# Kernel optimization log

Hardware: AMD Instinct MI355X
Metric: run time of the kernel (lower is better)

The kernel has to match this reference:

```python
import jax, jax.numpy as jnp
import numpy as np

B, N, D_IN, D_OUT = 8, 2048, 256, 128
ROW_ZERO = 85 - 10  # hardcoded in original: a[:, 0:85-10] = 0 (zeros rows, dim 1)
NEG_BIG = -9.0e15
EPS = 1e-12  # F.normalize eps


def setup_inputs() -> dict:
    key = jax.random.key(0)
    k1, k2, k3, k4 = jax.random.split(key, 4)
    h = jax.random.normal(k1, (B, N, D_IN), dtype=jnp.float32)
    adj = jax.random.randint(k2, (B, N, N), 0, 2, dtype=jnp.int32)
    adj_eye = jax.random.randint(k3, (B, N, N), 0, 2, dtype=jnp.int32)
    # xavier_uniform with gain=1.414 for W [in, out]
    limit = 1.414 * np.sqrt(6.0 / (D_IN + D_OUT))
    W = jax.random.uniform(k4, (D_IN, D_OUT), minval=-limit, maxval=limit, dtype=jnp.float32)
    return {"h": h, "adj": adj, "adj_eye": adj_eye, "W": W}


def reference(h, adj, adj_eye, W):
    # Wh: [B, N, D_OUT]
    Wh = jnp.matmul(h, W)
    # L2-normalize along feature dim (F.normalize semantics: x / max(||x||, eps))
    norm = jnp.maximum(jnp.linalg.norm(Wh, axis=-1, keepdims=True), EPS)
    Whn = Wh / norm
    # dense cosine-similarity scores: [B, N, N]
    score = jnp.einsum("bnd,bmd->bnm", Whn, Whn)
    # double-sort top-k emulation (faithful to original, incl. row-wise zeroing bug)
    a_sorted = jnp.sort(score, axis=-1)
    idx1 = jnp.argsort(score, axis=-1)
    a_sorted = a_sorted.at[:, 0:ROW_ZERO, :].set(0.0)
    idx2 = jnp.argsort(idx1, axis=-1)  # inverse permutation
    attscore = jnp.take_along_axis(a_sorted, idx2, axis=-1)
    # adjacency mask + softmax over neighbors
    e = jnp.where(adj_eye > 0, attscore, NEG_BIG)
    attention = jax.nn.softmax(e, axis=-1)
    # (dropout is identity in eval mode)
    h_prime = jnp.matmul(attention, Wh)
    return jax.nn.elu(h_prime)
```

## Files before the change

kernel.cpp:

```cpp
#include <hip/hip_runtime.h>
#include <stdint.h>

#define NN   2048
#define DD   128
#define DIN  256
#define ROWZ 75

typedef float f32x4 __attribute__((ext_vector_type(4)));
typedef short bf16x8 __attribute__((ext_vector_type(8)));
typedef unsigned int u32x4 __attribute__((ext_vector_type(4)));
typedef unsigned int u32x2 __attribute__((ext_vector_type(2)));
typedef unsigned long long u64x2 __attribute__((ext_vector_type(2)));

__device__ __forceinline__ unsigned short f2bf(float x){
  union { float f; unsigned int u; } v; v.f = x;
  unsigned int u = v.u;
  u += 0x7fffu + ((u >> 16) & 1u);
  return (unsigned short)(u >> 16);
}
__device__ __forceinline__ float bf2f(unsigned short b){
  union { float f; unsigned int u; } v; v.u = ((unsigned int)b) << 16;
  return v.f;
}

__launch_bounds__(256, 8)
__global__ void pack_kernel(const int* __restrict__ adje,
                            unsigned long long* __restrict__ adjp)
{
  const int t  = threadIdx.x;
  const int wv = t >> 6;
  const int ln = t & 63;
#pragma unroll
  for (int rr = 0; rr < 2; ++rr){
    const int row = blockIdx.x * 8 + wv * 2 + rr;
    const int* arow = adje + (size_t)row * NN;
    unsigned long long* drow = adjp + (size_t)row * 32;
#pragma unroll
    for (int c = 0; c < 4; ++c){
      int pv[8];
#pragma unroll
      for (int j = 0; j < 8; ++j) pv[j] = arow[c*512 + j*64 + ln];
      unsigned long long m[8];
#pragma unroll
      for (int j = 0; j < 8; ++j) m[j] = __ballot(pv[j] > 0);
      if (ln == 0){
#pragma unroll
        for (int j = 0; j < 8; j += 2){
          u64x2 pk = { m[j], m[j+1] };
          *(u64x2*)(drow + c*8 + j) = pk;
        }
      }
    }
  }
}

__launch_bounds__(256, 2)
__global__ void wh_kernel(const float* __restrict__ h, const float* __restrict__ W,
                          unsigned short* __restrict__ whn, unsigned short* __restrict__ whT)
{
  __shared__ float hs[32][36];
  __shared__ float Ws[32][128];
  __shared__ float ssp[32][33];
  __shared__ float sinv[32];

  const int t  = threadIdx.x;
  const int r0 = blockIdx.x * 32;
  const int r4 = (t >> 5) * 4;
  const int d4 = (t & 31) * 4;

  float acc[4][4];
#pragma unroll
  for (int i = 0; i < 4; ++i)
#pragma unroll
    for (int j = 0; j < 4; ++j) acc[i][j] = 0.f;

  const int lrow = t >> 3;
  const int lkb  = (t & 7) * 4;
  const int wk   = t >> 3;
  const int wd   = (t & 7) * 16;

  f32x4 ph = *(const f32x4*)(h + (size_t)(r0 + lrow) * DIN + lkb);
  f32x4 pW[4];
  {
    const float* ws = W + (size_t)wk * DD + wd;
#pragma unroll
    for (int e = 0; e < 4; ++e) pW[e] = ((const f32x4*)ws)[e];
  }

  for (int kt = 0; kt < 8; ++kt){
    __syncthreads();
#pragma unroll
    for (int e = 0; e < 4; ++e) hs[lkb + e][lrow] = ph[e];
    {
      f32x4* dst = (f32x4*)&Ws[wk][wd];
#pragma unroll
      for (int e = 0; e < 4; ++e) dst[e] = pW[e];
    }
    __syncthreads();

    if (kt < 7){
      ph = *(const f32x4*)(h + (size_t)(r0 + lrow) * DIN + (kt+1)*32 + lkb);
      const float* ws = W + (size_t)((kt+1)*32 + wk) * DD + wd;
#pragma unroll
      for (int e = 0; e < 4; ++e) pW[e] = ((const f32x4*)ws)[e];
    }

#pragma unroll
    for (int k = 0; k < 32; ++k){
      f32x4 w4 = *(const f32x4*)&Ws[k][d4];
      f32x4 ha = *(const f32x4*)&hs[k][r4];
#pragma unroll
      for (int i = 0; i < 4; ++i)
#pragma unroll
        for (int j = 0; j < 4; ++j)
          acc[i][j] += ha[i] * w4[j];
    }
  }

#pragma unroll
  for (int i = 0; i < 4; ++i){
    float s = acc[i][0]*acc[i][0] + acc[i][1]*acc[i][1]
            + acc[i][2]*acc[i][2] + acc[i][3]*acc[i][3];
    ssp[r4 + i][t & 31] = s;
  }
  __syncthreads();
  if (t < 32){
    float ss = 0.f;
#pragma unroll
    for (int c = 0; c < 32; ++c) ss += ssp[t][c];
    sinv[t] = 1.0f / fmaxf(sqrtf(ss), 1e-12f);
  }
  __syncthreads();

  const int bb = r0 >> 11;
  const int n0 = (r0 & 2047) + r4;

#pragma unroll
  for (int i = 0; i < 4; ++i){
    const float inv = sinv[r4 + i];
    unsigned int lo = (unsigned int)f2bf(acc[i][0]*inv) | ((unsigned int)f2bf(acc[i][1]*inv) << 16);
    unsigned int hi = (unsigned int)f2bf(acc[i][2]*inv) | ((unsigned int)f2bf(acc[i][3]*inv) << 16);
    u32x2 pk = { lo, hi };
    *(u32x2*)(whn + (size_t)(r0 + r4 + i) * DD + d4) = pk;
  }
#pragma unroll
  for (int j = 0; j < 4; ++j){
    u32x2 pk;
#pragma unroll
    for (int e = 0; e < 2; ++e)
      pk[e] = (unsigned int)f2bf(acc[2*e][j]) | ((unsigned int)f2bf(acc[2*e + 1][j]) << 16);
    *(u32x2*)(whT + ((size_t)(bb * DD + d4 + j)) * NN + n0) = pk;
  }
}

__launch_bounds__(256, 2)
__global__ void attn_kernel(const unsigned short* __restrict__ whn,
                            const unsigned short* __restrict__ whT,
                            const unsigned int* __restrict__ adjp,
                            float* __restrict__ out)
{
  __shared__ unsigned short Vt[2][128 * 128];
  __shared__ unsigned short Pbuf[4][32 * 40];
  __shared__ float linv_s[32];

  const int t    = threadIdx.x;
  const int w    = t >> 6;
  const int l    = t & 63;
  const int quad = l >> 4;
  const int l16  = l & 15;
  const int b     = blockIdx.x & 7;
  const int qbase = (blockIdx.x >> 3) * 32;

  const unsigned short* whn_b = whn + (size_t)b * NN * DD;
  const unsigned short* whT_b = whT + (size_t)b * DD * NN;
  const unsigned int*   adjw  = adjp + ((size_t)(b * NN + qbase)) * 64;

  bf16x8 qf[2][4];
#pragma unroll
  for (int s = 0; s < 2; ++s)
#pragma unroll
    for (int kc = 0; kc < 4; ++kc)
      qf[s][kc] = *(const bf16x8*)(whn_b + (size_t)(qbase + s*16 + l16) * DD + kc*32 + quad*8);

  f32x4 oacc[2][8];
  float lacc[2][4];
#pragma unroll
  for (int s = 0; s < 2; ++s){
#pragma unroll
    for (int dt = 0; dt < 8; ++dt) oacc[s][dt] = (f32x4){0.f, 0.f, 0.f, 0.f};
#pragma unroll
    for (int r = 0; r < 4; ++r) lacc[s][r] = 0.f;
  }

  unsigned short* const Pw = &Pbuf[w][0];

#pragma unroll
  for (int ii = 0; ii < 8; ++ii){
    const int d   = w*32 + ii*4 + quad;
    const int gsw = l16 ^ (d & 7);
    const unsigned short* src = whT_b + (size_t)d * NN + gsw * 8;
    __builtin_amdgcn_global_load_lds(
        (const __attribute__((address_space(1))) void*)src,
        (__attribute__((address_space(3))) void*)&Vt[0][(w*32 + ii*4) * 128],
        16, 0, 0);
  }
  unsigned int aw[2][4];
#pragma unroll
  for (int s = 0; s < 2; ++s)
#pragma unroll
    for (int r = 0; r < 4; ++r)
      aw[s][r] = adjw[(size_t)(s*16 + quad*4 + r) * 64 + w];

  for (int it = 0; it < 16; ++it){
    const int m0  = it * 128;
    const int cur = it & 1;

    bf16x8 kf[2][4];
#pragma unroll
    for (int f = 0; f < 2; ++f)
#pragma unroll
      for (int kc = 0; kc < 4; ++kc)
        kf[f][kc] = *(const bf16x8*)(whn_b + (size_t)(m0 + w*32 + f*16 + l16) * DD + kc*32 + quad*8);

    unsigned int awn[2][4];
    if (it < 15){
#pragma unroll
      for (int s = 0; s < 2; ++s)
#pragma unroll
        for (int r = 0; r < 4; ++r)
          awn[s][r] = adjw[(size_t)(s*16 + quad*4 + r) * 64 + (it+1)*4 + w];
#pragma unroll
      for (int ii = 0; ii < 8; ++ii){
        const int d   = w*32 + ii*4 + quad;
        const int gsw = l16 ^ (d & 7);
        const unsigned short* src = whT_b + (size_t)d * NN + (m0 + 128) + gsw * 8;
        __builtin_amdgcn_global_load_lds(
            (const __attribute__((address_space(1))) void*)src,
            (__attribute__((address_space(3))) void*)&Vt[cur ^ 1][(w*32 + ii*4) * 128],
            16, 0, 0);
      }
    }

#pragma unroll
    for (int f = 0; f < 2; ++f){
#pragma unroll
      for (int s = 0; s < 2; ++s){
        f32x4 sc = (f32x4){0.f, 0.f, 0.f, 0.f};
#pragma unroll
        for (int kc = 0; kc < 4; ++kc)
          sc = __builtin_amdgcn_mfma_f32_16x16x32_bf16(qf[s][kc], kf[f][kc], sc, 0, 0, 0);
#pragma unroll
        for (int r = 0; r < 4; ++r){
          const int qrow = qbase + s*16 + quad*4 + r;
          float sv = (qrow < ROWZ) ? 0.f : sc[r];
          float p32 = ((aw[s][r] >> (f*16 + l16)) & 1u) ? __expf(sv) : 0.f;
          unsigned short pb = f2bf(p32);
          lacc[s][r] += bf2f(pb);
          Pw[(s*16 + quad*4 + r) * 40 + f*16 + l16] = pb;
        }
      }
    }

    __builtin_amdgcn_sched_barrier(0);
    __builtin_amdgcn_s_barrier();
    __builtin_amdgcn_sched_barrier(0);

    bf16x8 pfr0 = *(const bf16x8*)&Pw[(l16) * 40 + quad*8];
    bf16x8 pfr1 = *(const bf16x8*)&Pw[(16 + l16) * 40 + quad*8];
    __builtin_amdgcn_s_setprio(1);
#pragma unroll
    for (int dt = 0; dt < 8; ++dt){
      const int d  = dt*16 + l16;
      const int gg = (w*4 + quad) ^ (d & 7);
      bf16x8 vf = *(const bf16x8*)&Vt[cur][d * 128 + gg * 8];
      oacc[0][dt] = __builtin_amdgcn_mfma_f32_16x16x32_bf16(pfr0, vf, oacc[0][dt], 0, 0, 0);
      oacc[1][dt] = __builtin_amdgcn_mfma_f32_16x16x32_bf16(pfr1, vf, oacc[1][dt], 0, 0, 0);
    }
    __builtin_amdgcn_s_setprio(0);

    __builtin_amdgcn_sched_barrier(0);
    __builtin_amdgcn_s_barrier();
    __builtin_amdgcn_sched_barrier(0);

    if (it < 15){
#pragma unroll
      for (int s = 0; s < 2; ++s)
#pragma unroll
        for (int r = 0; r < 4; ++r)
          aw[s][r] = awn[s][r];
    }
  }

  {
    float* lredw = (float*)Pw;
#pragma unroll
    for (int s = 0; s < 2; ++s)
#pragma unroll
      for (int r = 0; r < 4; ++r)
        lredw[(s*16 + quad*4 + r) * 16 + l16] = lacc[s][r];
  }
  __syncthreads();
  if (t < 32){
    float sum = 0.f;
    for (int ww = 0; ww < 4; ++ww){
      const float* lr = (const float*)&Pbuf[ww][0];
#pragma unroll
      for (int c = 0; c < 16; ++c) sum += lr[t * 16 + c];
    }
    linv_s[t] = 1.0f / sum;
  }

  float* const ored = (float*)&Vt[0][0];
  for (int s = 0; s < 2; ++s){
    __syncthreads();
#pragma unroll
    for (int dt = 0; dt < 8; ++dt)
#pragma unroll
      for (int r = 0; r < 4; ++r)
        ored[w*2048 + (quad*4 + r)*128 + dt*16 + l16] = oacc[s][dt][r];
    __syncthreads();
#pragma unroll
    for (int j = 0; j < 8; ++j){
      const int o  = j*256 + t;
      const int ql = o >> 7, d = o & 127;
      float v = ored[ql*128 + d] + ored[2048 + ql*128 + d]
              + ored[4096 + ql*128 + d] + ored[6144 + ql*128 + d];
      v *= linv_s[s*16 + ql];
      v = (v > 0.f) ? v : expm1f(v);
      out[(size_t)(b*NN + qbase + s*16 + ql) * DD + d] = v;
    }
  }
}

extern "C" void kernel_launch(void* const* d_in, const int* in_sizes, int n_in,
                              void* d_out, int out_size, void* d_ws, size_t ws_size,
                              hipStream_t stream)
{
  const float* h       = (const float*)d_in[0];
  const int*   adj_eye = (const int*)d_in[2];
  const float* W       = (const float*)d_in[3];
  float*       out     = (float*)d_out;

  unsigned short* whn  = (unsigned short*)d_ws;
  unsigned short* whT  = whn + (size_t)16384 * 128;
  unsigned int*   adjp = (unsigned int*)(whT + (size_t)16384 * 128);

  pack_kernel<<<2048, 256, 0, stream>>>(adj_eye, (unsigned long long*)adjp);
  wh_kernel<<<512, 256, 0, stream>>>(h, W, whn, whT);
  attn_kernel<<<512, 256, 0, stream>>>(whn, whT, adjp, out);
}
```

Before: 329.8 us.

## Fuse adjacency packing into attention kernel and stage K tiles in LDS

Drops the separate pack kernel; the attention kernel now reads the int32 adjacency directly, prefetching it one tile ahead in registers. Blocks grow to 512 threads covering 64 query rows, with half the waves staging K tiles and half staging V tiles into double-buffered LDS through direct global-to-LDS loads. The wh kernel's block-to-row mapping is interleaved across batches. The aim is to remove a kernel launch and the write and reread of a packed bitmask, and to share K/V tiles across more query rows. In exchange each block reads 4-byte adjacency values instead of packed bits, and the larger LDS footprint may lower occupancy.

```diff
diff --git a/kernel.cpp b/kernel.cpp
--- a/kernel.cpp
+++ b/kernel.cpp
@@ -8,9 +8,7 @@
 
 typedef float f32x4 __attribute__((ext_vector_type(4)));
 typedef short bf16x8 __attribute__((ext_vector_type(8)));
-typedef unsigned int u32x4 __attribute__((ext_vector_type(4)));
 typedef unsigned int u32x2 __attribute__((ext_vector_type(2)));
-typedef unsigned long long u64x2 __attribute__((ext_vector_type(2)));
 
 __device__ __forceinline__ unsigned short f2bf(float x){
   union { float f; unsigned int u; } v; v.f = x;
@@ -21,37 +19,6 @@
 __device__ __forceinline__ float bf2f(unsigned short b){
   union { float f; unsigned int u; } v; v.u = ((unsigned int)b) << 16;
   return v.f;
-}
-
-__launch_bounds__(256, 8)
-__global__ void pack_kernel(const int* __restrict__ adje,
-                            unsigned long long* __restrict__ adjp)
-{
-  const int t  = threadIdx.x;
-  const int wv = t >> 6;
-  const int ln = t & 63;
-#pragma unroll
-  for (int rr = 0; rr < 2; ++rr){
-    const int row = blockIdx.x * 8 + wv * 2 + rr;
-    const int* arow = adje + (size_t)row * NN;
-    unsigned long long* drow = adjp + (size_t)row * 32;
-#pragma unroll
-    for (int c = 0; c < 4; ++c){
-      int pv[8];
-#pragma unroll
-      for (int j = 0; j < 8; ++j) pv[j] = arow[c*512 + j*64 + ln];
-      unsigned long long m[8];
-#pragma unroll
-      for (int j = 0; j < 8; ++j) m[j] = __ballot(pv[j] > 0);
-      if (ln == 0){
-#pragma unroll
-        for (int j = 0; j < 8; j += 2){
-          u64x2 pk = { m[j], m[j+1] };
-          *(u64x2*)(drow + c*8 + j) = pk;
-        }
-      }
-    }
-  }
 }
 
 __launch_bounds__(256, 2)
@@ -64,7 +31,8 @@
   __shared__ float sinv[32];
 
   const int t  = threadIdx.x;
-  const int r0 = blockIdx.x * 32;
+  const int bid = blockIdx.x;
+  const int r0 = ((bid & 7) << 11) | ((bid >> 3) << 5);
   const int r4 = (t >> 5) * 4;
   const int d4 = (t & 31) * 4;
 
@@ -153,34 +121,62 @@
   }
 }
 
-__launch_bounds__(256, 2)
+__launch_bounds__(512, 2)
 __global__ void attn_kernel(const unsigned short* __restrict__ whn,
                             const unsigned short* __restrict__ whT,
-                            const unsigned int* __restrict__ adjp,
+                            const int* __restrict__ adje,
                             float* __restrict__ out)
 {
+  __shared__ unsigned short Kt[2][128 * 128];
   __shared__ unsigned short Vt[2][128 * 128];
-  __shared__ unsigned short Pbuf[4][32 * 40];
-  __shared__ float linv_s[32];
+  __shared__ unsigned short Pbuf[8][32 * 40];
+  __shared__ float linv_s[64];
 
   const int t    = threadIdx.x;
   const int w    = t >> 6;
   const int l    = t & 63;
   const int quad = l >> 4;
   const int l16  = l & 15;
+  const int qh   = w >> 2;
+  const int ms   = w & 3;
   const int b     = blockIdx.x & 7;
-  const int qbase = (blockIdx.x >> 3) * 32;
+  const int qbase = (blockIdx.x >> 3) * 64;
 
   const unsigned short* whn_b = whn + (size_t)b * NN * DD;
   const unsigned short* whT_b = whT + (size_t)b * DD * NN;
-  const unsigned int*   adjw  = adjp + ((size_t)(b * NN + qbase)) * 64;
+  const int*            adj_b = adje + (size_t)b * NN * NN;
+
+#define STAGE(M0, CC)                                                          \
+  if (w < 4){                                                                  \
+    _Pragma("unroll")                                                          \
+    for (int ii = 0; ii < 8; ++ii){                                            \
+      const int row = w*32 + ii*4 + (l >> 4);                                  \
+      const unsigned short* src = whn_b + (size_t)((M0) + row) * DD            \
+                                  + (l16 ^ (row & 7)) * 8;                     \
+      __builtin_amdgcn_global_load_lds(                                        \
+          (const __attribute__((address_space(1))) void*)src,                  \
+          (__attribute__((address_space(3))) void*)&Kt[CC][(w*32 + ii*4)*128], \
+          16, 0, 0);                                                           \
+    }                                                                          \
+  } else {                                                                     \
+    _Pragma("unroll")                                                          \
+    for (int ii = 0; ii < 8; ++ii){                                            \
+      const int dv = (w-4)*32 + ii*4 + (l >> 4);                               \
+      const unsigned short* src = whT_b + (size_t)dv * NN + (M0)               \
+                                  + (l16 ^ (dv & 7)) * 8;                      \
+      __builtin_amdgcn_global_load_lds(                                        \
+          (const __attribute__((address_space(1))) void*)src,                  \
+          (__attribute__((address_space(3))) void*)&Vt[CC][((w-4)*32+ii*4)*128],\
+          16, 0, 0);                                                           \
+    }                                                                          \
+  }
 
   bf16x8 qf[2][4];
 #pragma unroll
   for (int s = 0; s < 2; ++s)
 #pragma unroll
     for (int kc = 0; kc < 4; ++kc)
-      qf[s][kc] = *(const bf16x8*)(whn_b + (size_t)(qbase + s*16 + l16) * DD + kc*32 + quad*8);
+      qf[s][kc] = *(const bf16x8*)(whn_b + (size_t)(qbase + qh*32 + s*16 + l16) * DD + kc*32 + quad*8);
 
   f32x4 oacc[2][8];
   float lacc[2][4];
@@ -194,53 +190,42 @@
 
   unsigned short* const Pw = &Pbuf[w][0];
 
-#pragma unroll
-  for (int ii = 0; ii < 8; ++ii){
-    const int d   = w*32 + ii*4 + quad;
-    const int gsw = l16 ^ (d & 7);
-    const unsigned short* src = whT_b + (size_t)d * NN + gsw * 8;
-    __builtin_amdgcn_global_load_lds(
-        (const __attribute__((address_space(1))) void*)src,
-        (__attribute__((address_space(3))) void*)&Vt[0][(w*32 + ii*4) * 128],
-        16, 0, 0);
-  }
-  unsigned int aw[2][4];
-#pragma unroll
-  for (int s = 0; s < 2; ++s)
-#pragma unroll
-    for (int r = 0; r < 4; ++r)
-      aw[s][r] = adjw[(size_t)(s*16 + quad*4 + r) * 64 + w];
+  int av[2][2][4];
+#pragma unroll
+  for (int f = 0; f < 2; ++f)
+#pragma unroll
+    for (int s = 0; s < 2; ++s)
+#pragma unroll
+      for (int r = 0; r < 4; ++r)
+        av[f][s][r] = adj_b[(size_t)(qbase + qh*32 + s*16 + quad*4 + r) * NN + ms*32 + f*16 + l16];
+  STAGE(0, 0)
+  __syncthreads();
 
   for (int it = 0; it < 16; ++it){
     const int m0  = it * 128;
     const int cur = it & 1;
 
+    int avn[2][2][4];
+    if (it < 15){
+      const int mn = m0 + 128;
+#pragma unroll
+      for (int f = 0; f < 2; ++f)
+#pragma unroll
+        for (int s = 0; s < 2; ++s)
+#pragma unroll
+          for (int r = 0; r < 4; ++r)
+            avn[f][s][r] = adj_b[(size_t)(qbase + qh*32 + s*16 + quad*4 + r) * NN + mn + ms*32 + f*16 + l16];
+      STAGE(mn, cur ^ 1)
+    }
+
     bf16x8 kf[2][4];
 #pragma unroll
     for (int f = 0; f < 2; ++f)
 #pragma unroll
-      for (int kc = 0; kc < 4; ++kc)
-        kf[f][kc] = *(const bf16x8*)(whn_b + (size_t)(m0 + w*32 + f*16 + l16) * DD + kc*32 + quad*8);
-
-    unsigned int awn[2][4];
-    if (it < 15){
-#pragma unroll
-      for (int s = 0; s < 2; ++s)
-#pragma unroll
-        for (int r = 0; r < 4; ++r)
-          awn[s][r] = adjw[(size_t)(s*16 + quad*4 + r) * 64 + (it+1)*4 + w];
-#pragma unroll
-      for (int ii = 0; ii < 8; ++ii){
-        const int d   = w*32 + ii*4 + quad;
-        const int gsw = l16 ^ (d & 7);
-        const unsigned short* src = whT_b + (size_t)d * NN + (m0 + 128) + gsw * 8;
-        __builtin_amdgcn_global_load_lds(
-            (const __attribute__((address_space(1))) void*)src,
-            (__attribute__((address_space(3))) void*)&Vt[cur ^ 1][(w*32 + ii*4) * 128],
-            16, 0, 0);
+      for (int kc = 0; kc < 4; ++kc){
+        const int row = ms*32 + f*16 + l16;
+        kf[f][kc] = *(const bf16x8*)&Kt[cur][row*128 + (((kc*4 + quad) ^ (l16 & 7)) * 8)];
       }
-    }
-
 #pragma unroll
     for (int f = 0; f < 2; ++f){
 #pragma unroll
@@ -251,9 +236,9 @@
           sc = __builtin_amdgcn_mfma_f32_16x16x32_bf16(qf[s][kc], kf[f][kc], sc, 0, 0, 0);
 #pragma unroll
         for (int r = 0; r < 4; ++r){
-          const int qrow = qbase + s*16 + quad*4 + r;
+          const int qrow = qbase + qh*32 + s*16 + quad*4 + r;
           float sv = (qrow < ROWZ) ? 0.f : sc[r];
-          float p32 = ((aw[s][r] >> (f*16 + l16)) & 1u) ? __expf(sv) : 0.f;
+          float p32 = (av[f][s][r] > 0) ? __expf(sv) : 0.f;
           unsigned short pb = f2bf(p32);
           lacc[s][r] += bf2f(pb);
           Pw[(s*16 + quad*4 + r) * 40 + f*16 + l16] = pb;
@@ -261,75 +246,79 @@
       }
     }
 
+    bf16x8 pfr0 = *(const bf16x8*)&Pw[(l16) * 40 + quad*8];
+    bf16x8 pfr1 = *(const bf16x8*)&Pw[(16 + l16) * 40 + quad*8];
+    __builtin_amdgcn_s_setprio(1);
+#pragma unroll
+    for (int dt = 0; dt < 8; ++dt){
+      const int d = dt*16 + l16;
+      bf16x8 vf = *(const bf16x8*)&Vt[cur][d*128 + (((ms*4 + quad) ^ (l16 & 7)) * 8)];
+      oacc[0][dt] = __builtin_amdgcn_mfma_f32_16x16x32_bf16(pfr0, vf, oacc[0][dt], 0, 0, 0);
+      oacc[1][dt] = __builtin_amdgcn_mfma_f32_16x16x32_bf16(pfr1, vf, oacc[1][dt], 0, 0, 0);
+    }
+    __builtin_amdgcn_s_setprio(0);
+
+    __builtin_amdgcn_sched_barrier(0);
+    asm volatile("s_waitcnt vmcnt(0)" ::: "memory");
     __builtin_amdgcn_sched_barrier(0);
     __builtin_amdgcn_s_barrier();
     __builtin_amdgcn_sched_barrier(0);
 
-    bf16x8 pfr0 = *(const bf16x8*)&Pw[(l16) * 40 + quad*8];
-    bf16x8 pfr1 = *(const bf16x8*)&Pw[(16 + l16) * 40 + quad*8];
-    __builtin_amdgcn_s_setprio(1);
-#pragma unroll
-    for (int dt = 0; dt < 8; ++dt){
-      const int d  = dt*16 + l16;
-      const int gg = (w*4 + quad) ^ (d & 7);
-      bf16x8 vf = *(const bf16x8*)&Vt[cur][d * 128 + gg * 8];
-      oacc[0][dt] = __builtin_amdgcn_mfma_f32_16x16x32_bf16(pfr0, vf, oacc[0][dt], 0, 0, 0);
-      oacc[1][dt] = __builtin_amdgcn_mfma_f32_16x16x32_bf16(pfr1, vf, oacc[1][dt], 0, 0, 0);
-    }
-    __builtin_amdgcn_s_setprio(0);
-
-    __builtin_amdgcn_sched_barrier(0);
-    __builtin_amdgcn_s_barrier();
-    __builtin_amdgcn_sched_barrier(0);
-
     if (it < 15){
 #pragma unroll
-      for (int s = 0; s < 2; ++s)
-#pragma unroll
-        for (int r = 0; r < 4; ++r)
-          aw[s][r] = awn[s][r];
+      for (int f = 0; f < 2; ++f)
+#pragma unroll
+        for (int s = 0; s < 2; ++s)
+#pragma unroll
+          for (int r = 0; r < 4; ++r)
+            av[f][s][r] = avn[f][s][r];
     }
   }
 
   {
-    float* lredw = (float*)Pw;
+    float* fl = (float*)&Pbuf[0][0];
 #pragma unroll
     for (int s = 0; s < 2; ++s)
 #pragma unroll
       for (int r = 0; r < 4; ++r)
-        lredw[(s*16 + quad*4 + r) * 16 + l16] = lacc[s][r];
+        fl[(qh*32 + s*16 + quad*4 + r) * 64 + ms*16 + l16] = lacc[s][r];
   }
   __syncthreads();
-  if (t < 32){
+  if (t < 64){
+    const float* fl = (const float*)&Pbuf[0][0];
     float sum = 0.f;
-    for (int ww = 0; ww < 4; ++ww){
-      const float* lr = (const float*)&Pbuf[ww][0];
-#pragma unroll
-      for (int c = 0; c < 16; ++c) sum += lr[t * 16 + c];
-    }
+#pragma unroll
+    for (int c = 0; c < 64; ++c) sum += fl[t * 64 + c];
     linv_s[t] = 1.0f / sum;
   }
 
-  float* const ored = (float*)&Vt[0][0];
+  float* const owf = (float*)&Kt[0][0];
   for (int s = 0; s < 2; ++s){
     __syncthreads();
 #pragma unroll
     for (int dt = 0; dt < 8; ++dt)
 #pragma unroll
       for (int r = 0; r < 4; ++r)
-        ored[w*2048 + (quad*4 + r)*128 + dt*16 + l16] = oacc[s][dt][r];
+        owf[w*2048 + (quad*4 + r)*128 + dt*16 + l16] = oacc[s][dt][r];
     __syncthreads();
 #pragma unroll
     for (int j = 0; j < 8; ++j){
-      const int o  = j*256 + t;
-      const int ql = o >> 7, d = o & 127;
-      float v = ored[ql*128 + d] + ored[2048 + ql*128 + d]
-              + ored[4096 + ql*128 + d] + ored[6144 + ql*128 + d];
-      v *= linv_s[s*16 + ql];
+      const int o     = j*512 + t;
+      const int row32 = o >> 7;
+      const int d     = o & 127;
+      const int qh2   = row32 >> 4;
+      const int r16   = row32 & 15;
+      float v = owf[(qh2*4 + 0)*2048 + r16*128 + d]
+              + owf[(qh2*4 + 1)*2048 + r16*128 + d]
+              + owf[(qh2*4 + 2)*2048 + r16*128 + d]
+              + owf[(qh2*4 + 3)*2048 + r16*128 + d];
+      const int qrl = qh2*32 + s*16 + r16;
+      v *= linv_s[qrl];
       v = (v > 0.f) ? v : expm1f(v);
-      out[(size_t)(b*NN + qbase + s*16 + ql) * DD + d] = v;
-    }
-  }
+      out[(size_t)(b*NN + qbase + qrl) * DD + d] = v;
+    }
+  }
+#undef STAGE
 }
 
 extern "C" void kernel_launch(void* const* d_in, const int* in_sizes, int n_in,
@@ -343,9 +332,7 @@
 
   unsigned short* whn  = (unsigned short*)d_ws;
   unsigned short* whT  = whn + (size_t)16384 * 128;
-  unsigned int*   adjp = (unsigned int*)(whT + (size_t)16384 * 128);
-
-  pack_kernel<<<2048, 256, 0, stream>>>(adj_eye, (unsigned long long*)adjp);
+
   wh_kernel<<<512, 256, 0, stream>>>(h, W, whn, whT);
-  attn_kernel<<<512, 256, 0, stream>>>(whn, whT, adjp, out);
-}
+  attn_kernel<<<256, 512, 0, stream>>>(whn, whT, adj_eye, out);
+}
```

After: 285.8 us. 13.3% less time.
